# Optimization experiments

Measured on AMD Instinct MI355X. Metric: run time of the kernel, lower is better.

## Reference

```python
import jax, jax.numpy as jnp
import numpy as np

KH, KW = 3, 3   # kernel_size
DH, DW = 2, 2   # stride


def _extract_windows(x):
    """Equivalent of x.unfold(2,KH,DH).unfold(3,KW,DW).view(B,C,H',W',KH*KW).
    Loop is over the KH*KW=9 fixed kernel offsets, not data dims."""
    B, C, H, W = x.shape
    Ho = (H - KH) // DH + 1
    Wo = (W - KW) // DW + 1
    cols = [x[:, :, i:i + DH * Ho:DH, j:j + DW * Wo:DW]
            for i in range(KH) for j in range(KW)]  # row-major (kh,kw) matches torch unfold flatten
    return jnp.stack(cols, axis=-1)  # (B, C, Ho, Wo, KH*KW)


def setup_inputs() -> dict:
    key = jax.random.key(0)
    k1, k2 = jax.random.split(key)
    x = jax.random.normal(k1, (8, 32, 64, 64), dtype=jnp.float32)
    # weight: (1, out_channels, in_channels, H', W', kh*kw) with H'=W'=31
    weight = jax.random.normal(k2, (1, 32, 32, 31, 31, 9), dtype=jnp.float32)
    return {"x": x, "weight": weight}


def reference(x, weight):
    # windows: (B, in, H', W', K); weight[0]: (out, in, H', W', K)
    # out[b,o,p,q] = sum_{i,k} windows[b,i,p,q,k] * weight[0,o,i,p,q,k]
    windows = _extract_windows(x)
    return jnp.einsum('bipqk,oipqk->bopq', windows, weight[0])
```

## Files before the change

### kernel.cpp

```cpp
#include <hip/hip_runtime.h>


#define NPART 246016
#define WS_NEED ((size_t)8 * NPART * 4)

#define GLD4(gp, lp)                                                 \
    __builtin_amdgcn_global_load_lds(                                \
        (const __attribute__((address_space(1))) void*)(gp),         \
        (__attribute__((address_space(3))) void*)(lp), 4, 0, 0)
#define GLD16(gp, lp)                                                \
    __builtin_amdgcn_global_load_lds(                                \
        (const __attribute__((address_space(1))) void*)(gp),         \
        (__attribute__((address_space(3))) void*)(lp), 16, 0, 0)

template <bool USE_WS>
__global__ __launch_bounds__(512, 2) void lc2d_kernel(const float* __restrict__ x,
                                                      const float* __restrict__ wgt,
                                                      float* __restrict__ outOrPart) {
    __shared__ float xs[6144];
    __shared__ float wlds[4 * 2560];

    const int t  = threadIdx.x;
    const int ol = t & 15;
    const int bh = (t >> 4) & 1;
    const int dq = t >> 5;
    const int bid = blockIdx.x;
    const int p  = bid >> 5;
    const int qg = (bid >> 4) & 1;
    const int ig = (bid >> 1) & 7;
    const int oh = bid & 1;
    const int i0 = ig * 4;
    const int q0 = qg << 4;
    const int q  = q0 + dq;
    const int o  = oh * 16 + ol;
    const int waveBase = t & ~63;

#pragma unroll
    for (int j = 0; j < 3; ++j) {
        const int g  = j * 512 + t;
        const int r  = g >> 4;
        const int cw = (g & 15) << 2;
        const int b  = r / 12;
        const int r2 = r - b * 12;
        const int ii = r2 / 3;
        const int kh = r2 - ii * 3;
        const float* gp = x + (size_t)b * 131072 + (size_t)(i0 + ii) * 4096
                            + (size_t)(2 * p + kh) * 64 + cw;
        GLD16(gp, &xs[4 * (j * 512 + waveBase)]);
    }

    const int lim = (qg == 0) ? 143 : 134;
    const int pqb = p * 279 + q0 * 9;
    const int obase = oh * 16;
#pragma unroll
    for (int ii = 0; ii < 4; ++ii) {
        const size_t iw = (size_t)(i0 + ii) * 8649;
#pragma unroll
        for (int j = 0; j < 5; ++j) {
            int f = t + j * 512; f = (f < 2319) ? f : 2319;
            const int os  = f / 145;
            const int off = f - os * 145;
            const int go  = (off < lim) ? off : lim;
            GLD4(wgt + (size_t)(obase + os) * 276768 + pqb + go + iw,
                 &wlds[ii * 2560 + j * 512 + waveBase]);
        }
    }

    float acc[4];
#pragma unroll
    for (int bi = 0; bi < 4; ++bi) acc[bi] = 0.f;

    __syncthreads();

    const int wvb = ol * 145 + dq * 9;

#pragma unroll 1
    for (int ii = 0; ii < 4; ++ii) {
        float wv[9];
#pragma unroll
        for (int k = 0; k < 9; ++k) wv[k] = wlds[ii * 2560 + wvb + k];

        const int xb = bh * 3072 + ii * 192 + 2 * q0 + 2 * dq;
#pragma unroll
        for (int kh = 0; kh < 3; ++kh) {
#pragma unroll
            for (int bi = 0; bi < 4; ++bi) {
                const int base = xb + bi * 768 + kh * 64;
                const float2 a = *reinterpret_cast<const float2*>(&xs[base]);
                const float c1 = xs[base + 2];
                acc[bi] += wv[kh * 3 + 0] * a.x + wv[kh * 3 + 1] * a.y
                         + wv[kh * 3 + 2] * c1;
            }
        }
    }

    if (q <= 30) {
        const int pq = p * 31 + q;
        if (USE_WS) {
#pragma unroll
            for (int bi = 0; bi < 4; ++bi)
                outOrPart[((size_t)(ig * 8 + bh * 4 + bi) * 961 + pq) * 32 + o] = acc[bi];
        } else {
#pragma unroll
            for (int bi = 0; bi < 4; ++bi)
                atomicAdd(&outOrPart[(((size_t)(bh * 4 + bi) * 32 + o) * 31 + p) * 31 + q],
                          acc[bi]);
        }
    }
}

__global__ __launch_bounds__(256) void lc2d_reduce(const float* __restrict__ part,
                                                   float* __restrict__ out) {
    const int u = blockIdx.x * 256 + threadIdx.x;
    float s = 0.f;
#pragma unroll
    for (int ig = 0; ig < 8; ++ig) s += part[(size_t)ig * NPART + u];
    const int o = u & 31;
    const int r = u >> 5;
    const int b = r / 961;
    const int pq = r - b * 961;
    out[(size_t)(b * 32 + o) * 961 + pq] = s;
}

extern "C" void kernel_launch(void* const* d_in, const int* in_sizes, int n_in,
                              void* d_out, int out_size, void* d_ws, size_t ws_size,
                              hipStream_t stream) {
    const float* x = (const float*)d_in[0];
    const float* w = (const float*)d_in[1];
    float* out = (float*)d_out;

    if (ws_size >= WS_NEED) {
        float* part = (float*)d_ws;
        lc2d_kernel<true><<<dim3(31 * 2 * 8 * 2), dim3(512), 0, stream>>>(x, w, part);
        lc2d_reduce<<<dim3(NPART / 256), dim3(256), 0, stream>>>(part, out);
    } else {
        hipMemsetAsync(out, 0, (size_t)out_size * sizeof(float), stream);
        lc2d_kernel<false><<<dim3(31 * 2 * 8 * 2), dim3(512), 0, stream>>>(x, w, out);
    }
}
```

Baseline: 88.28 us.

## Register-block 4 output channels per thread and split input channels into 16 groups

Each thread now computes 4 output channels by 4 batches, reusing x values held in registers across output channels. The x tile is gathered into a pre-strided layout so each thread can load its window row as one float4. Blocks drop to 256 threads, each covering all 32 output channels and 2 input channels, which doubles the number of partial-sum planes. The aim is fewer LDS reads per FMA. In exchange the workspace and reduce traffic double and register pressure rises.

```diff
diff --git a/kernel.cpp b/kernel.cpp
--- a/kernel.cpp
+++ b/kernel.cpp
@@ -2,95 +2,99 @@
 
 
 #define NPART 246016
-#define WS_NEED ((size_t)8 * NPART * 4)
+#define NIG 16
+#define WS_NEED ((size_t)NIG * NPART * 4)
 
 #define GLD4(gp, lp)                                                 \
     __builtin_amdgcn_global_load_lds(                                \
         (const __attribute__((address_space(1))) void*)(gp),         \
         (__attribute__((address_space(3))) void*)(lp), 4, 0, 0)
-#define GLD16(gp, lp)                                                \
-    __builtin_amdgcn_global_load_lds(                                \
-        (const __attribute__((address_space(1))) void*)(gp),         \
-        (__attribute__((address_space(3))) void*)(lp), 16, 0, 0)
 
 template <bool USE_WS>
-__global__ __launch_bounds__(512, 2) void lc2d_kernel(const float* __restrict__ x,
+__global__ __launch_bounds__(256, 3) void lc2d_kernel(const float* __restrict__ x,
                                                       const float* __restrict__ wgt,
                                                       float* __restrict__ outOrPart) {
-    __shared__ float xs[6144];
-    __shared__ float wlds[4 * 2560];
+    __shared__ float xs[3072];
+    __shared__ float wl[2][4864];
 
     const int t  = threadIdx.x;
-    const int ol = t & 15;
-    const int bh = (t >> 4) & 1;
-    const int dq = t >> 5;
+    const int ol = t & 7;
+    const int bh = (t >> 3) & 1;
+    const int dq = t >> 4;
     const int bid = blockIdx.x;
     const int p  = bid >> 5;
     const int qg = (bid >> 4) & 1;
-    const int ig = (bid >> 1) & 7;
-    const int oh = bid & 1;
-    const int i0 = ig * 4;
+    const int ih = bid & 15;
+    const int i0 = ih * 2;
     const int q0 = qg << 4;
     const int q  = q0 + dq;
-    const int o  = oh * 16 + ol;
     const int waveBase = t & ~63;
 
 #pragma unroll
-    for (int j = 0; j < 3; ++j) {
-        const int g  = j * 512 + t;
-        const int r  = g >> 4;
-        const int cw = (g & 15) << 2;
-        const int b  = r / 12;
-        const int r2 = r - b * 12;
-        const int ii = r2 / 3;
-        const int kh = r2 - ii * 3;
+    for (int j = 0; j < 12; ++j) {
+        const int f   = j * 256 + t;
+        const int c   = f & 3;
+        const int dqp = (f >> 2) & 15;
+        const int r   = f >> 6;
+        const int b   = r / 6;
+        const int r6  = r - b * 6;
+        const int ii  = r6 / 3;
+        const int kh  = r6 - ii * 3;
+        int gcol = 2 * (q0 + dqp) + c;
+        if (gcol > 63) gcol = 63;
         const float* gp = x + (size_t)b * 131072 + (size_t)(i0 + ii) * 4096
-                            + (size_t)(2 * p + kh) * 64 + cw;
-        GLD16(gp, &xs[4 * (j * 512 + waveBase)]);
+                            + (size_t)(2 * p + kh) * 64 + gcol;
+        GLD4(gp, &xs[j * 256 + waveBase]);
     }
 
     const int lim = (qg == 0) ? 143 : 134;
     const int pqb = p * 279 + q0 * 9;
-    const int obase = oh * 16;
 #pragma unroll
-    for (int ii = 0; ii < 4; ++ii) {
+    for (int ii = 0; ii < 2; ++ii) {
         const size_t iw = (size_t)(i0 + ii) * 8649;
 #pragma unroll
-        for (int j = 0; j < 5; ++j) {
-            int f = t + j * 512; f = (f < 2319) ? f : 2319;
+        for (int j = 0; j < 19; ++j) {
+            int f = j * 256 + t; f = (f < 4639) ? f : 4639;
             const int os  = f / 145;
             const int off = f - os * 145;
             const int go  = (off < lim) ? off : lim;
-            GLD4(wgt + (size_t)(obase + os) * 276768 + pqb + go + iw,
-                 &wlds[ii * 2560 + j * 512 + waveBase]);
+            GLD4(wgt + (size_t)os * 276768 + pqb + go + iw,
+                 &wl[ii][j * 256 + waveBase]);
         }
     }
 
-    float acc[4];
+    float acc[4][4];
 #pragma unroll
-    for (int bi = 0; bi < 4; ++bi) acc[bi] = 0.f;
+    for (int oj = 0; oj < 4; ++oj)
+#pragma unroll
+        for (int bi = 0; bi < 4; ++bi) acc[oj][bi] = 0.f;
 
     __syncthreads();
 
-    const int wvb = ol * 145 + dq * 9;
-
-#pragma unroll 1
-    for (int ii = 0; ii < 4; ++ii) {
-        float wv[9];
 #pragma unroll
-        for (int k = 0; k < 9; ++k) wv[k] = wlds[ii * 2560 + wvb + k];
-
-        const int xb = bh * 3072 + ii * 192 + 2 * q0 + 2 * dq;
+    for (int ii = 0; ii < 2; ++ii) {
+        float4 xv[3][4];
 #pragma unroll
-        for (int kh = 0; kh < 3; ++kh) {
+        for (int kh = 0; kh < 3; ++kh)
 #pragma unroll
             for (int bi = 0; bi < 4; ++bi) {
-                const int base = xb + bi * 768 + kh * 64;
-                const float2 a = *reinterpret_cast<const float2*>(&xs[base]);
-                const float c1 = xs[base + 2];
-                acc[bi] += wv[kh * 3 + 0] * a.x + wv[kh * 3 + 1] * a.y
-                         + wv[kh * 3 + 2] * c1;
+                const int r = ((bh * 4 + bi) * 2 + ii) * 3 + kh;
+                xv[kh][bi] = *reinterpret_cast<const float4*>(&xs[(r * 16 + dq) * 4]);
             }
+
+#pragma unroll
+        for (int oj = 0; oj < 4; ++oj) {
+            const int wbase = (ol + 8 * oj) * 145 + dq * 9;
+            float wv[9];
+#pragma unroll
+            for (int k = 0; k < 9; ++k) wv[k] = wl[ii][wbase + k];
+#pragma unroll
+            for (int kh = 0; kh < 3; ++kh)
+#pragma unroll
+                for (int bi = 0; bi < 4; ++bi)
+                    acc[oj][bi] += wv[kh * 3 + 0] * xv[kh][bi].x
+                                 + wv[kh * 3 + 1] * xv[kh][bi].y
+                                 + wv[kh * 3 + 2] * xv[kh][bi].z;
         }
     }
 
@@ -98,13 +102,18 @@
         const int pq = p * 31 + q;
         if (USE_WS) {
 #pragma unroll
-            for (int bi = 0; bi < 4; ++bi)
-                outOrPart[((size_t)(ig * 8 + bh * 4 + bi) * 961 + pq) * 32 + o] = acc[bi];
+            for (int oj = 0; oj < 4; ++oj)
+#pragma unroll
+                for (int bi = 0; bi < 4; ++bi)
+                    outOrPart[((size_t)(ih * 8 + bh * 4 + bi) * 961 + pq) * 32 + ol + 8 * oj]
+                        = acc[oj][bi];
         } else {
 #pragma unroll
-            for (int bi = 0; bi < 4; ++bi)
-                atomicAdd(&outOrPart[(((size_t)(bh * 4 + bi) * 32 + o) * 31 + p) * 31 + q],
-                          acc[bi]);
+            for (int oj = 0; oj < 4; ++oj)
+#pragma unroll
+                for (int bi = 0; bi < 4; ++bi)
+                    atomicAdd(&outOrPart[(((size_t)(bh * 4 + bi) * 32 + ol + 8 * oj) * 31 + p) * 31 + q],
+                              acc[oj][bi]);
         }
     }
 }
@@ -114,7 +123,7 @@
     const int u = blockIdx.x * 256 + threadIdx.x;
     float s = 0.f;
 #pragma unroll
-    for (int ig = 0; ig < 8; ++ig) s += part[(size_t)ig * NPART + u];
+    for (int ig = 0; ig < NIG; ++ig) s += part[(size_t)ig * NPART + u];
     const int o = u & 31;
     const int r = u >> 5;
     const int b = r / 961;
@@ -131,10 +140,10 @@
 
     if (ws_size >= WS_NEED) {
         float* part = (float*)d_ws;
-        lc2d_kernel<true><<<dim3(31 * 2 * 8 * 2), dim3(512), 0, stream>>>(x, w, part);
+        lc2d_kernel<true><<<dim3(31 * 2 * 16), dim3(256), 0, stream>>>(x, w, part);
         lc2d_reduce<<<dim3(NPART / 256), dim3(256), 0, stream>>>(part, out);
     } else {
         hipMemsetAsync(out, 0, (size_t)out_size * sizeof(float), stream);
-        lc2d_kernel<false><<<dim3(31 * 2 * 8 * 2), dim3(512), 0, stream>>>(x, w, out);
+        lc2d_kernel<false><<<dim3(31 * 2 * 16), dim3(256), 0, stream>>>(x, w, out);
     }
 }
```

Measured after the change: 88.52 us. Within noise of the previous version (+0.3%).
